# Optimization experiments

Measured on AMD Instinct MI355X. Metric: run time of the kernel, lower is better.

Reference implementation:

```python
import jax, jax.numpy as jnp
import numpy as np


def setup_inputs() -> dict:
    key = jax.random.key(0)
    ks = jax.random.split(key, 5)
    N, C, H, W = 4, 256, 64, 64
    fan_scale = 1.0 / np.sqrt(C)  # kaiming-ish scale for 1x1 conv weights
    x = jax.random.normal(ks[0], (N, C, H, W), dtype=jnp.float32)
    Wq = jax.random.normal(ks[1], (C, C), dtype=jnp.float32) * fan_scale
    Wk = jax.random.normal(ks[2], (C, C), dtype=jnp.float32) * fan_scale
    Wv = jax.random.normal(ks[3], (C, C), dtype=jnp.float32) * fan_scale
    bq = jnp.zeros((C,), dtype=jnp.float32)
    bk = jnp.zeros((C,), dtype=jnp.float32)
    bv = jnp.zeros((C,), dtype=jnp.float32)
    gamma = jax.random.uniform(ks[4], (1,), dtype=jnp.float32)
    return {"x": x, "Wq": Wq, "bq": bq, "Wk": Wk, "bk": bk, "Wv": Wv, "bv": bv, "gamma": gamma}


def reference(x, Wq, bq, Wk, bk, Wv, bv, gamma):
    # x: (N, C, H, W); 1x1 convs are channel-mixing matmuls.
    N, C, H, W = x.shape
    HW = H * W
    xf = x.reshape(N, C, HW)
    q = jnp.einsum('oc,ncl->nol', Wq, xf) + bq[None, :, None]  # (N, C, HW)
    k = jnp.einsum('oc,ncl->nol', Wk, xf) + bk[None, :, None]
    v = jnp.einsum('oc,ncl->nol', Wv, xf) + bv[None, :, None]
    # spatial mode: energy = softmax(Q^T K) over last dim (no 1/sqrt(d) scaling)
    energy = jax.nn.softmax(jnp.einsum('nci,ncj->nij', q, k), axis=-1)  # (N, HW, HW)
    # att[n,c,i] = sum_j v[n,c,j] * energy[n,i,j]  (bmm(value, energy^T))
    att = jnp.einsum('ncj,nij->nci', v, energy)  # (N, C, HW)
    # in_channels == out_channels -> residual is identity
    out = x + gamma[0] * att.reshape(N, C, H, W)
    return out
```

## Files before the change

### kernel.cpp

```cpp
#include <hip/hip_runtime.h>

typedef unsigned short ushort_t;
typedef unsigned int u32;
typedef _Float16 f16;
typedef f16 f16x8 __attribute__((ext_vector_type(8)));
typedef f16 f16x2 __attribute__((ext_vector_type(2)));
typedef ushort_t u16x8 __attribute__((ext_vector_type(8)));
typedef float f32x4 __attribute__((ext_vector_type(4)));
typedef float f32x16 __attribute__((ext_vector_type(16)));

#define C_DIM 256
#define HW 4096
#define CHW (C_DIM*HW)
#define L2E 1.4426950408889634f

__device__ __align__(16) f16 g_xbT[4 * CHW];
__device__ __align__(16) f16 g_q[4 * CHW];
__device__ __align__(16) f16 g_k[4 * CHW];
__device__ __align__(16) f16 g_v[4 * CHW];
__device__ __align__(16) f16 g_opart[16 * CHW];
__device__ __align__(16) float g_ml[16 * 2 * HW];

__device__ __forceinline__ float bf2f(ushort_t h) {
    union { u32 u; float f; } v; v.u = ((u32)h) << 16; return v.f;
}
__device__ __forceinline__ ushort_t f2bf(float f) {
    union { float f; u32 u; } v; v.f = f;
    u32 r = v.u + 0x7FFF + ((v.u >> 16) & 1);
    return (ushort_t)(r >> 16);
}
__device__ __forceinline__ float fin0(float v) {
    return (v > -1e30f && v < 1e30f) ? v : 0.f;
}
__device__ __forceinline__ f16 sf16(float v) {
    return (f16)((v > -1e4f && v < 1e4f) ? v : 0.f);
}
__device__ __forceinline__ void gl2lds16(const f16* g, f16* l) {
    __builtin_amdgcn_global_load_lds(
        (const __attribute__((address_space(1))) u32*)g,
        (__attribute__((address_space(3))) u32*)l, 16, 0, 0);
}
__device__ __forceinline__ int probe_mode(const void* p) {
    int lane = threadIdx.x & 63;
    float v = fabsf(bf2f(((const ushort_t*)p)[lane]));
    v = (v < 1e6f) ? v : 1e6f;
#pragma unroll
    for (int d = 1; d < 64; d <<= 1) v += __shfl_xor(v, d, 64);
    return (v * (1.f / 64.f) > 100.f) ? 1 : 0;
}

__global__ void k_sentinel(ushort_t* out, int n) {
    int i = blockIdx.x * 256 + threadIdx.x;
    if (i < n) out[i] = f2bf(777.f);
}

__global__ __launch_bounds__(256) void k_transpose(const void* __restrict__ xv) {
    __shared__ f16 t[64][66];
    int mode = probe_mode(xv);
    int n = blockIdx.z, c0 = blockIdx.y * 64, l0 = blockIdx.x * 64;
    int tid = threadIdx.x;
    f16* ob = g_xbT + n * CHW;
    int lq = (tid & 15) * 4;
    int cl = tid >> 4;
    if (mode == 0) {
        const ushort_t* xb = (const ushort_t*)xv + n * CHW;
#pragma unroll
        for (int p = 0; p < 4; ++p) {
            int c = cl + 16 * p;
            ushort4 v = *(const ushort4*)(xb + (c0 + c) * HW + l0 + lq);
            t[lq + 0][c] = sf16(bf2f(v.x));
            t[lq + 1][c] = sf16(bf2f(v.y));
            t[lq + 2][c] = sf16(bf2f(v.z));
            t[lq + 3][c] = sf16(bf2f(v.w));
        }
    } else {
        const float* xb = (const float*)xv + n * CHW;
#pragma unroll
        for (int p = 0; p < 4; ++p) {
            int c = cl + 16 * p;
            float4 v = *(const float4*)(xb + (c0 + c) * HW + l0 + lq);
            t[lq + 0][c] = sf16(v.x);
            t[lq + 1][c] = sf16(v.y);
            t[lq + 2][c] = sf16(v.z);
            t[lq + 3][c] = sf16(v.w);
        }
    }
    __syncthreads();
    int c2 = (tid & 31) * 2;
    int lr = tid >> 5;
#pragma unroll
    for (int p = 0; p < 8; ++p) {
        int l = lr + 8 * p;
        u32 pair = *(const u32*)&t[l][c2];
        *(u32*)(ob + (l0 + l) * C_DIM + c0 + c2) = pair;
    }
}

__global__ __launch_bounds__(256) void k_proj(
    const void* __restrict__ Wq, const void* __restrict__ bq,
    const void* __restrict__ Wk, const void* __restrict__ bk,
    const void* __restrict__ Wv, const void* __restrict__ bv)
{
    __shared__ __align__(16) f16 lds_x[128 * 64];
    __shared__ __align__(16) f16 lds_w[128 * 64];
    int l0 = blockIdx.x * 128;
    int og0 = blockIdx.y * 128;
    int n = blockIdx.z;
    int mat = og0 >> 8;
    int om0 = og0 & 255;
    const void* W = (mat == 0) ? Wq : (mat == 1) ? Wk : Wv;
    const void* bias = (mat == 0) ? bq : (mat == 1) ? bk : bv;
    int mode = probe_mode(W);
    int tid = threadIdx.x, w = tid >> 6, lane = tid & 63;
    int quad = lane >> 4, l16 = lane & 15;
    const f16* xb = g_xbT + n * CHW;

    f32x4 acc[2][8];
#pragma unroll
    for (int a = 0; a < 2; a++)
#pragma unroll
        for (int b = 0; b < 8; b++) acc[a][b] = f32x4{0.f, 0.f, 0.f, 0.f};

    for (int ch = 0; ch < 4; ++ch) {
        int cc0 = ch * 64;
        f16x8 xs[4], wsr[4];
#pragma unroll
        for (int ti = 0; ti < 4; ++ti) {
            int s = (w * 4 + ti) * 64 + lane;
            int row = s >> 3, gp = s & 7;
            xs[ti] = *(const f16x8*)(xb + (l0 + row) * C_DIM + cc0 + gp * 8);
            f16x8 h;
            if (mode == 0) {
                u16x8 wv = *(const u16x8*)((const ushort_t*)W + (om0 + row) * C_DIM + cc0 + gp * 8);
#pragma unroll
                for (int e = 0; e < 8; e++) h[e] = sf16(bf2f(wv[e]));
            } else {
                const float* wf = (const float*)W + (om0 + row) * C_DIM + cc0 + gp * 8;
#pragma unroll
                for (int e = 0; e < 8; e++) h[e] = sf16(wf[e]);
            }
            wsr[ti] = h;
        }
        __syncthreads();
#pragma unroll
        for (int ti = 0; ti < 4; ++ti) {
            int s = (w * 4 + ti) * 64 + lane;
            int row = s >> 3, gp = s & 7;
            int pos = gp ^ (row & 7);
            *(f16x8*)(lds_x + (row * 8 + pos) * 8) = xs[ti];
            *(f16x8*)(lds_w + (row * 8 + pos) * 8) = wsr[ti];
        }
        __syncthreads();
#pragma unroll
        for (int ks = 0; ks < 2; ++ks) {
            f16x8 af[2];
#pragma unroll
            for (int mt = 0; mt < 2; ++mt) {
                int row = w * 32 + mt * 16 + l16;
                int g = ks * 4 + quad;
                int pos = g ^ (row & 7);
                af[mt] = *(const f16x8*)(lds_x + (row * 8 + pos) * 8);
            }
#pragma unroll
            for (int nt = 0; nt < 8; ++nt) {
                int rowo = nt * 16 + l16;
                int g = ks * 4 + quad;
                int pos = g ^ (rowo & 7);
                f16x8 bfv = *(const f16x8*)(lds_w + (rowo * 8 + pos) * 8);
                if (mat < 2) {
                    acc[0][nt] = __builtin_amdgcn_mfma_f32_16x16x32_f16(af[0], bfv, acc[0][nt], 0, 0, 0);
                    acc[1][nt] = __builtin_amdgcn_mfma_f32_16x16x32_f16(af[1], bfv, acc[1][nt], 0, 0, 0);
                } else {
                    acc[0][nt] = __builtin_amdgcn_mfma_f32_16x16x32_f16(bfv, af[0], acc[0][nt], 0, 0, 0);
                    acc[1][nt] = __builtin_amdgcn_mfma_f32_16x16x32_f16(bfv, af[1], acc[1][nt], 0, 0, 0);
                }
            }
        }
        __syncthreads();
    }

    auto loadb = [&](int i) -> float {
        return mode ? ((const float*)bias)[i] : bf2f(((const ushort_t*)bias)[i]);
    };
    if (mat < 2) {
        f16* T = ((mat == 0) ? g_q : g_k) + n * CHW;
        float bvv[8];
#pragma unroll
        for (int nt = 0; nt < 8; nt++) bvv[nt] = loadb(om0 + nt * 16 + l16);
#pragma unroll
        for (int mt = 0; mt < 2; mt++)
#pragma unroll
            for (int nt = 0; nt < 8; nt++)
#pragma unroll
                for (int r = 0; r < 4; r++) {
                    int l = l0 + w * 32 + mt * 16 + quad * 4 + r;
                    int o = om0 + nt * 16 + l16;
                    T[l * C_DIM + o] = sf16(acc[mt][nt][r] + bvv[nt]);
                }
    } else {
        f16* T = g_v + n * CHW;
#pragma unroll
        for (int mt = 0; mt < 2; mt++)
#pragma unroll
            for (int nt = 0; nt < 8; nt++)
#pragma unroll
                for (int r = 0; r < 4; r++) {
                    int o = om0 + nt * 16 + quad * 4 + r;
                    int l = l0 + w * 32 + mt * 16 + l16;
                    T[o * HW + l] = sf16(acc[mt][nt][r] + loadb(o));
                }
    }
}

__device__ __forceinline__ f16x8 pack_pfrag(const float* p, int h) {
    union PK { u32 u; f16x2 h2; } t0, t1, t2, t3;
    t0.h2 = f16x2{(f16)p[0], (f16)p[1]};
    t1.h2 = f16x2{(f16)p[2], (f16)p[3]};
    t2.h2 = f16x2{(f16)p[4], (f16)p[5]};
    t3.h2 = f16x2{(f16)p[6], (f16)p[7]};
    u32 sa = __shfl_xor(t0.u, 32, 64);
    u32 sb = __shfl_xor(t1.u, 32, 64);
    u32 sc = __shfl_xor(t2.u, 32, 64);
    u32 sd = __shfl_xor(t3.u, 32, 64);
    union RW { u32 w[4]; f16x8 v; } r;
    r.w[0] = h ? sc : t0.u;
    r.w[1] = h ? sd : t1.u;
    r.w[2] = h ? t2.u : sa;
    r.w[3] = h ? t3.u : sb;
    return r.v;
}

__global__ __launch_bounds__(256, 2) void k_attn() {
    __shared__ __align__(16) f16 smem[40960];
    f16* kbuf = smem;
    f16* vbuf = smem + 16384;

    int bid = blockIdx.x;
    int x8 = bid & 7;
    int n = x8 >> 1, jhi = x8 & 1;
    int rest = bid >> 3;
    int jlo = rest & 1;
    int i0 = (rest >> 1) * 128;
    int jq = jhi * 2 + jlo;
    int tid = threadIdx.x, w = tid >> 6, lane = tid & 63;
    int j5 = lane & 31, h = lane >> 5;

    const f16* Qb = g_q + n * CHW;
    const f16* Kb = g_k + n * CHW;
    const f16* Vb = g_v + n * CHW;

    f16x8 qf[16];
    {
        const f16* qrow = Qb + (i0 + w * 32 + j5) * C_DIM + h * 8;
#pragma unroll
        for (int ck = 0; ck < 16; ++ck)
            qf[ck] = *(const f16x8*)(qrow + ck * 16);
    }

    int k_lane = h * 256 + j5 * 8;
    int v_lane = h * 2048 + j5 * 8;

    const f16* ksrc = Kb + (jq * 1024 + j5) * C_DIM + (w * 2 + h) * 8;
    const f16* vsrc = Vb + tid * HW + jq * 1024;
    int dst_w = w * 512;

    f32x16 o_acc[8];
#pragma unroll
    for (int ct = 0; ct < 8; ++ct)
#pragma unroll
        for (int r = 0; r < 16; ++r) o_acc[ct][r] = 0.f;

    float m_ = -1e30f, l_ = 0.f, al_prev = 1.f;
    f16x8 pf0 = {}, pf1 = {};

#pragma unroll
    for (int s = 0; s < 4; ++s) gl2lds16(ksrc + s * 64, kbuf + s * 2048 + dst_w);
    ksrc += 32 * C_DIM;
#pragma unroll
    for (int s = 0; s < 4; ++s) gl2lds16(vsrc + s * 8, vbuf + s * 2048 + dst_w);
    vsrc += 32;
    __syncthreads();

    int vs_stage = 1, vs_pv = 2;
    for (int it = 0; it < 32; ++it) {
        int kb_cur = it & 1;
        if (it < 31) {
#pragma unroll
            for (int s = 0; s < 4; ++s)
                gl2lds16(ksrc + s * 64, kbuf + (kb_cur ^ 1) * 8192 + s * 2048 + dst_w);
            ksrc += 32 * C_DIM;
#pragma unroll
            for (int s = 0; s < 4; ++s)
                gl2lds16(vsrc + s * 8, vbuf + vs_stage * 8192 + s * 2048 + dst_w);
            vsrc += 32;
        }

        const f16* kb = kbuf + kb_cur * 8192 + k_lane;
        f32x16 st;
#pragma unroll
        for (int r = 0; r < 16; ++r) st[r] = 0.f;
        __builtin_amdgcn_s_setprio(1);
#pragma unroll
        for (int ck = 0; ck < 16; ++ck) {
            f16x8 kf = *(const f16x8*)(kb + ck * 512);
            st = __builtin_amdgcn_mfma_f32_32x32x16_f16(kf, qf[ck], st, 0, 0, 0);
        }

        if (it > 0) {
            if (__any(al_prev < 1.f)) {
#pragma unroll
                for (int ct = 0; ct < 8; ++ct)
#pragma unroll
                    for (int r = 0; r < 16; ++r) o_acc[ct][r] *= al_prev;
            }
            const f16* vb = vbuf + vs_pv * 8192 + v_lane;
#pragma unroll
            for (int ct = 0; ct < 8; ++ct) {
                f16x8 v0 = *(const f16x8*)(vb + ct * 256);
                f16x8 v1 = *(const f16x8*)(vb + 4096 + ct * 256);
                o_acc[ct] = __builtin_amdgcn_mfma_f32_32x32x16_f16(v0, pf0, o_acc[ct], 0, 0, 0);
                o_acc[ct] = __builtin_amdgcn_mfma_f32_32x32x16_f16(v1, pf1, o_acc[ct], 0, 0, 0);
            }
        }
        __builtin_amdgcn_s_setprio(0);

        float mx0 = fmaxf(fmaxf(st[0], st[1]), fmaxf(st[2], st[3]));
        float mx1 = fmaxf(fmaxf(st[4], st[5]), fmaxf(st[6], st[7]));
        float mx2 = fmaxf(fmaxf(st[8], st[9]), fmaxf(st[10], st[11]));
        float mx3 = fmaxf(fmaxf(st[12], st[13]), fmaxf(st[14], st[15]));
        float smax = fmaxf(fmaxf(mx0, mx1), fmaxf(mx2, mx3));
        smax = fmaxf(smax, __shfl_xor(smax, 32, 64));
        float mq = __builtin_ceilf(smax * 0.125f) * 8.f;
        float mn = fmaxf(m_, mq);
        float al = __builtin_amdgcn_exp2f((m_ - mn) * L2E);
        float nl = -mn * L2E;
        float p[16];
#pragma unroll
        for (int r = 0; r < 16; ++r)
            p[r] = __builtin_amdgcn_exp2f(st[r] * L2E + nl);
        float a0 = (p[0] + p[1]) + (p[2] + p[3]);
        float a1 = (p[4] + p[5]) + (p[6] + p[7]);
        float a2 = (p[8] + p[9]) + (p[10] + p[11]);
        float a3 = (p[12] + p[13]) + (p[14] + p[15]);
        float rs = (a0 + a1) + (a2 + a3);
        rs += __shfl_xor(rs, 32, 64);
        m_ = mn;
        l_ = l_ * al + rs;
        al_prev = al;
        pf0 = pack_pfrag(p, h);
        pf1 = pack_pfrag(p + 8, h);

        __syncthreads();
        vs_pv = (vs_pv == 2) ? 0 : vs_pv + 1;
        vs_stage = (vs_stage == 2) ? 0 : vs_stage + 1;
    }

    {
        if (__any(al_prev < 1.f)) {
#pragma unroll
            for (int ct = 0; ct < 8; ++ct)
#pragma unroll
                for (int r = 0; r < 16; ++r) o_acc[ct][r] *= al_prev;
        }
        const f16* vb = vbuf + vs_pv * 8192 + v_lane;
#pragma unroll
        for (int ct = 0; ct < 8; ++ct) {
            f16x8 v0 = *(const f16x8*)(vb + ct * 256);
            f16x8 v1 = *(const f16x8*)(vb + 4096 + ct * 256);
            o_acc[ct] = __builtin_amdgcn_mfma_f32_32x32x16_f16(v0, pf0, o_acc[ct], 0, 0, 0);
            o_acc[ct] = __builtin_amdgcn_mfma_f32_32x32x16_f16(v1, pf1, o_acc[ct], 0, 0, 0);
        }
    }

    int slot = jq * 4 + n;
    int i_out = i0 + w * 32 + j5;
    if (h == 0) {
        g_ml[(slot * 2 + 0) * HW + i_out] = m_;
        g_ml[(slot * 2 + 1) * HW + i_out] = l_;
    }
    float inv = (l_ > 1e-30f) ? 1.f / l_ : 0.f;
    f16* ob = g_opart + slot * CHW + i_out;
#pragma unroll
    for (int ct = 0; ct < 8; ++ct) {
        int cbase = ct * 32 + 4 * h;
#pragma unroll
        for (int r = 0; r < 16; ++r) {
            int c = cbase + (r & 3) + 8 * (r >> 2);
            ob[c * HW] = (f16)(o_acc[ct][r] * inv);
        }
    }
}

__global__ __launch_bounds__(256) void k_combine(
    const void* __restrict__ xv, const void* __restrict__ gv, void* __restrict__ outv)
{
    int mode = probe_mode(xv);
    float gam = fin0(mode ? ((const float*)gv)[0] : bf2f(((const ushort_t*)gv)[0]));
    int n = blockIdx.y;
    int off = blockIdx.x * 2048 + threadIdx.x * 8;
    int i = off & (HW - 1);

    u16x8 op[4];
    float ms[4][8], ls[4][8];
#pragma unroll
    for (int s = 0; s < 4; ++s) {
        int slot = s * 4 + n;
        op[s] = *(const u16x8*)((const ushort_t*)g_opart + slot * CHW + off);
        float4 mA = *(const float4*)&g_ml[(slot * 2 + 0) * HW + i];
        float4 mB = *(const float4*)&g_ml[(slot * 2 + 0) * HW + i + 4];
        float4 lA = *(const float4*)&g_ml[(slot * 2 + 1) * HW + i];
        float4 lB = *(const float4*)&g_ml[(slot * 2 + 1) * HW + i + 4];
        ms[s][0]=mA.x; ms[s][1]=mA.y; ms[s][2]=mA.z; ms[s][3]=mA.w;
        ms[s][4]=mB.x; ms[s][5]=mB.y; ms[s][6]=mB.z; ms[s][7]=mB.w;
        ls[s][0]=lA.x; ls[s][1]=lA.y; ls[s][2]=lA.z; ls[s][3]=lA.w;
        ls[s][4]=lB.x; ls[s][5]=lB.y; ls[s][6]=lB.z; ls[s][7]=lB.w;
    }

    float o[8];
#pragma unroll
    for (int e = 0; e < 8; ++e) {
        float m = fmaxf(fmaxf(ms[0][e], ms[1][e]), fmaxf(ms[2][e], ms[3][e]));
        float num = 0.f, den = 0.f;
#pragma unroll
        for (int s = 0; s < 4; ++s) {
            float wgt = __builtin_amdgcn_exp2f((ms[s][e] - m) * L2E) * ls[s][e];
            union { ushort_t u; f16 h; } cv; cv.u = (ushort_t)op[s][e];
            num += wgt * (float)cv.h;
            den += wgt;
        }
        o[e] = (den > 1e-30f) ? num / den : 0.f;
    }

    if (mode == 0) {
        u16x8 xp = *(const u16x8*)((const ushort_t*)xv + n * CHW + off);
        u16x8 res;
#pragma unroll
        for (int e = 0; e < 8; ++e)
            res[e] = f2bf(fin0(bf2f((ushort_t)xp[e]) + gam * o[e]));
        *(u16x8*)((ushort_t*)outv + n * CHW + off) = res;
    } else {
        const float* xb = (const float*)xv + n * CHW + off;
        float* outb = (float*)outv + n * CHW + off;
        float4 xA = *(const float4*)xb;
        float4 xB = *(const float4*)(xb + 4);
        float4 rA, rB;
        rA.x = fin0(xA.x + gam * o[0]); rA.y = fin0(xA.y + gam * o[1]);
        rA.z = fin0(xA.z + gam * o[2]); rA.w = fin0(xA.w + gam * o[3]);
        rB.x = fin0(xB.x + gam * o[4]); rB.y = fin0(xB.y + gam * o[5]);
        rB.z = fin0(xB.z + gam * o[6]); rB.w = fin0(xB.w + gam * o[7]);
        *(float4*)outb = rA;
        *(float4*)(outb + 4) = rB;
    }
}

extern "C" void kernel_launch(void* const* d_in, const int* in_sizes, int n_in,
                              void* d_out, int out_size, void* d_ws, size_t ws_size,
                              hipStream_t stream) {
    (void)d_ws; (void)ws_size;
    bool ok = (n_in == 8) &&
              in_sizes[0] == 4 * CHW &&
              in_sizes[1] == C_DIM * C_DIM && in_sizes[2] == C_DIM &&
              in_sizes[3] == C_DIM * C_DIM && in_sizes[4] == C_DIM &&
              in_sizes[5] == C_DIM * C_DIM && in_sizes[6] == C_DIM &&
              in_sizes[7] == 1 && out_size == 4 * CHW;
    if (!ok) {
        hipLaunchKernelGGL(k_sentinel, dim3((out_size + 255) / 256), dim3(256), 0, stream,
                           (ushort_t*)d_out, out_size);
        return;
    }
    hipLaunchKernelGGL(k_transpose, dim3(64, 4, 4), dim3(256), 0, stream, d_in[0]);
    hipLaunchKernelGGL(k_proj, dim3(32, 6, 4), dim3(256), 0, stream,
                       d_in[1], d_in[2], d_in[3], d_in[4], d_in[5], d_in[6]);
    hipLaunchKernelGGL(k_attn, dim3(512), dim3(256), 0, stream);
    hipLaunchKernelGGL(k_combine, dim3(CHW / 2048, 4), dim3(256), 0, stream,
                       d_in[0], d_in[7], d_out);
}
```

Baseline: 239.9 us.

## Interleave QK and PV MFMAs per step with double-buffered V tiles

The attention loop now issues the QK^T MFMAs and the previous step's PV MFMAs interleaved in a single loop. The score accumulator is split into two independent chains that are summed afterwards. The V staging buffer drops from three stages to two, shrinking LDS, and the V load now happens in the same iteration as its tile is consumed one step later. The cross-half row-sum shuffle moves out of the loop and runs once at the end. The aim is to hide MFMA dependency latency and cut per-iteration shuffle work, at the cost of higher register pressure and less slack between V loads and their use.

New measurement: 239.3 us. Within noise of the previous version (-0.2%).

```diff
diff --git a/kernel.cpp b/kernel.cpp
--- a/kernel.cpp
+++ b/kernel.cpp
@@ -231,7 +231,7 @@
 }
 
 __global__ __launch_bounds__(256, 2) void k_attn() {
-    __shared__ __align__(16) f16 smem[40960];
+    __shared__ __align__(16) f16 smem[32768];
     f16* kbuf = smem;
     f16* vbuf = smem + 16384;
 
@@ -276,53 +276,56 @@
 #pragma unroll
     for (int s = 0; s < 4; ++s) gl2lds16(ksrc + s * 64, kbuf + s * 2048 + dst_w);
     ksrc += 32 * C_DIM;
-#pragma unroll
-    for (int s = 0; s < 4; ++s) gl2lds16(vsrc + s * 8, vbuf + s * 2048 + dst_w);
-    vsrc += 32;
     __syncthreads();
 
-    int vs_stage = 1, vs_pv = 2;
     for (int it = 0; it < 32; ++it) {
-        int kb_cur = it & 1;
+        int kcur = it & 1;
         if (it < 31) {
 #pragma unroll
             for (int s = 0; s < 4; ++s)
-                gl2lds16(ksrc + s * 64, kbuf + (kb_cur ^ 1) * 8192 + s * 2048 + dst_w);
+                gl2lds16(ksrc + s * 64, kbuf + (kcur ^ 1) * 8192 + s * 2048 + dst_w);
             ksrc += 32 * C_DIM;
-#pragma unroll
-            for (int s = 0; s < 4; ++s)
-                gl2lds16(vsrc + s * 8, vbuf + vs_stage * 8192 + s * 2048 + dst_w);
-            vsrc += 32;
-        }
-
-        const f16* kb = kbuf + kb_cur * 8192 + k_lane;
+        }
+#pragma unroll
+        for (int s = 0; s < 4; ++s)
+            gl2lds16(vsrc + s * 8, vbuf + (it & 1) * 8192 + s * 2048 + dst_w);
+        vsrc += 32;
+
+        if (it > 0 && __any(al_prev < 1.f)) {
+#pragma unroll
+            for (int ct = 0; ct < 8; ++ct)
+#pragma unroll
+                for (int r = 0; r < 16; ++r) o_acc[ct][r] *= al_prev;
+        }
+
+        const f16* kb = kbuf + kcur * 8192 + k_lane;
+        f32x16 sa, sb;
+#pragma unroll
+        for (int r = 0; r < 16; ++r) { sa[r] = 0.f; sb[r] = 0.f; }
+        __builtin_amdgcn_s_setprio(1);
+        if (it > 0) {
+            const f16* vb = vbuf + ((it - 1) & 1) * 8192 + v_lane;
+#pragma unroll
+            for (int ck = 0; ck < 16; ++ck) {
+                f16x8 kf = *(const f16x8*)(kb + ck * 512);
+                if (ck & 1) sb = __builtin_amdgcn_mfma_f32_32x32x16_f16(kf, qf[ck], sb, 0, 0, 0);
+                else        sa = __builtin_amdgcn_mfma_f32_32x32x16_f16(kf, qf[ck], sa, 0, 0, 0);
+                f16x8 vf = *(const f16x8*)(vb + (ck & 1) * 4096 + (ck >> 1) * 256);
+                o_acc[ck >> 1] = __builtin_amdgcn_mfma_f32_32x32x16_f16(
+                    vf, (ck & 1) ? pf1 : pf0, o_acc[ck >> 1], 0, 0, 0);
+            }
+        } else {
+#pragma unroll
+            for (int ck = 0; ck < 16; ++ck) {
+                f16x8 kf = *(const f16x8*)(kb + ck * 512);
+                if (ck & 1) sb = __builtin_amdgcn_mfma_f32_32x32x16_f16(kf, qf[ck], sb, 0, 0, 0);
+                else        sa = __builtin_amdgcn_mfma_f32_32x32x16_f16(kf, qf[ck], sa, 0, 0, 0);
+            }
+        }
+        __builtin_amdgcn_s_setprio(0);
         f32x16 st;
 #pragma unroll
-        for (int r = 0; r < 16; ++r) st[r] = 0.f;
-        __builtin_amdgcn_s_setprio(1);
-#pragma unroll
-        for (int ck = 0; ck < 16; ++ck) {
-            f16x8 kf = *(const f16x8*)(kb + ck * 512);
-            st = __builtin_amdgcn_mfma_f32_32x32x16_f16(kf, qf[ck], st, 0, 0, 0);
-        }
-
-        if (it > 0) {
-            if (__any(al_prev < 1.f)) {
-#pragma unroll
-                for (int ct = 0; ct < 8; ++ct)
-#pragma unroll
-                    for (int r = 0; r < 16; ++r) o_acc[ct][r] *= al_prev;
-            }
-            const f16* vb = vbuf + vs_pv * 8192 + v_lane;
-#pragma unroll
-            for (int ct = 0; ct < 8; ++ct) {
-                f16x8 v0 = *(const f16x8*)(vb + ct * 256);
-                f16x8 v1 = *(const f16x8*)(vb + 4096 + ct * 256);
-                o_acc[ct] = __builtin_amdgcn_mfma_f32_32x32x16_f16(v0, pf0, o_acc[ct], 0, 0, 0);
-                o_acc[ct] = __builtin_amdgcn_mfma_f32_32x32x16_f16(v1, pf1, o_acc[ct], 0, 0, 0);
-            }
-        }
-        __builtin_amdgcn_s_setprio(0);
+        for (int r = 0; r < 16; ++r) st[r] = sa[r] + sb[r];
 
         float mx0 = fmaxf(fmaxf(st[0], st[1]), fmaxf(st[2], st[3]));
         float mx1 = fmaxf(fmaxf(st[4], st[5]), fmaxf(st[6], st[7]));
@@ -343,7 +346,6 @@
         float a2 = (p[8] + p[9]) + (p[10] + p[11]);
         float a3 = (p[12] + p[13]) + (p[14] + p[15]);
         float rs = (a0 + a1) + (a2 + a3);
-        rs += __shfl_xor(rs, 32, 64);
         m_ = mn;
         l_ = l_ * al + rs;
         al_prev = al;
@@ -351,8 +353,6 @@
         pf1 = pack_pfrag(p + 8, h);
 
         __syncthreads();
-        vs_pv = (vs_pv == 2) ? 0 : vs_pv + 1;
-        vs_stage = (vs_stage == 2) ? 0 : vs_stage + 1;
     }
 
     {
@@ -362,7 +362,7 @@
 #pragma unroll
                 for (int r = 0; r < 16; ++r) o_acc[ct][r] *= al_prev;
         }
-        const f16* vb = vbuf + vs_pv * 8192 + v_lane;
+        const f16* vb = vbuf + 8192 + v_lane;
 #pragma unroll
         for (int ct = 0; ct < 8; ++ct) {
             f16x8 v0 = *(const f16x8*)(vb + ct * 256);
@@ -371,6 +371,8 @@
             o_acc[ct] = __builtin_amdgcn_mfma_f32_32x32x16_f16(v1, pf1, o_acc[ct], 0, 0, 0);
         }
     }
+
+    l_ += __shfl_xor(l_, 32, 64);
 
     int slot = jq * 4 + n;
     int i_out = i0 + w * 32 + j5;
```

## Split attention channel dimension across wave pairs with LDS score exchange

Applied to the files above, without the earlier changes.

Each block now covers 64 query rows instead of 128, with pairs of waves splitting the 256 channels: each wave computes a partial QK^T over 128 channels, swaps partial scores with its peer through LDS, and accumulates PV for only half of the output channels. This halves the per-wave register footprint (qf and o_acc), which allows three blocks per CU, and doubles the grid size to improve occupancy and latency hiding. K and V staging drops from double/triple buffering to single buffers with explicit waitcnt and barriers, trading pipelining depth and extra synchronisation for lower LDS use. K/V are fetched once per 64 query rows instead of 128, so global and L2 traffic rises.

Measured after the change: 288.6 us. 20.3% more time.

```diff
diff --git a/kernel.cpp b/kernel.cpp
--- a/kernel.cpp
+++ b/kernel.cpp
@@ -230,43 +230,44 @@
     return r.v;
 }
 
-__global__ __launch_bounds__(256, 2) void k_attn() {
-    __shared__ __align__(16) f16 smem[40960];
+__global__ __launch_bounds__(256, 3) void k_attn() {
+    __shared__ __align__(16) f16 smem[24576];
     f16* kbuf = smem;
-    f16* vbuf = smem + 16384;
+    f16* vbuf = smem + 8192;
+    float* xbuf = (float*)(smem + 16384);
 
     int bid = blockIdx.x;
-    int x8 = bid & 7;
-    int n = x8 >> 1, jhi = x8 & 1;
-    int rest = bid >> 3;
-    int jlo = rest & 1;
-    int i0 = (rest >> 1) * 128;
-    int jq = jhi * 2 + jlo;
+    int n = bid & 3;
+    int jq = (bid >> 2) & 3;
+    int i0 = (bid >> 4) * 64;
     int tid = threadIdx.x, w = tid >> 6, lane = tid & 63;
     int j5 = lane & 31, h = lane >> 5;
+    int ic = w >> 1, ch = w & 1;
 
     const f16* Qb = g_q + n * CHW;
     const f16* Kb = g_k + n * CHW;
     const f16* Vb = g_v + n * CHW;
 
-    f16x8 qf[16];
+    f16x8 qf[8];
     {
-        const f16* qrow = Qb + (i0 + w * 32 + j5) * C_DIM + h * 8;
-#pragma unroll
-        for (int ck = 0; ck < 16; ++ck)
+        const f16* qrow = Qb + (i0 + ic * 32 + j5) * C_DIM + ch * 128 + h * 8;
+#pragma unroll
+        for (int ck = 0; ck < 8; ++ck)
             qf[ck] = *(const f16x8*)(qrow + ck * 16);
     }
 
-    int k_lane = h * 256 + j5 * 8;
-    int v_lane = h * 2048 + j5 * 8;
+    int k_lane = ch * 4096 + h * 256 + j5 * 8;
+    int v_lane = h * 2048 + ch * 1024 + j5 * 8;
+    float* x_my = xbuf + (ic * 2 + ch) * 1024 + lane * 16;
+    const float* x_peer = xbuf + (ic * 2 + (ch ^ 1)) * 1024 + lane * 16;
 
     const f16* ksrc = Kb + (jq * 1024 + j5) * C_DIM + (w * 2 + h) * 8;
     const f16* vsrc = Vb + tid * HW + jq * 1024;
     int dst_w = w * 512;
 
-    f32x16 o_acc[8];
-#pragma unroll
-    for (int ct = 0; ct < 8; ++ct)
+    f32x16 o_acc[4];
+#pragma unroll
+    for (int ct = 0; ct < 4; ++ct)
 #pragma unroll
         for (int r = 0; r < 16; ++r) o_acc[ct][r] = 0.f;
 
@@ -276,54 +277,71 @@
 #pragma unroll
     for (int s = 0; s < 4; ++s) gl2lds16(ksrc + s * 64, kbuf + s * 2048 + dst_w);
     ksrc += 32 * C_DIM;
-#pragma unroll
-    for (int s = 0; s < 4; ++s) gl2lds16(vsrc + s * 8, vbuf + s * 2048 + dst_w);
-    vsrc += 32;
-    __syncthreads();
-
-    int vs_stage = 1, vs_pv = 2;
+    asm volatile("s_waitcnt vmcnt(0)" ::: "memory");
+    __builtin_amdgcn_s_barrier();
+    __builtin_amdgcn_sched_barrier(0);
+
     for (int it = 0; it < 32; ++it) {
-        int kb_cur = it & 1;
+        if (it > 0) {
+            asm volatile("s_waitcnt vmcnt(4)" ::: "memory");
+            __builtin_amdgcn_s_barrier();
+            __builtin_amdgcn_sched_barrier(0);
+        }
+
+        const f16* kb = kbuf + k_lane;
+        f32x16 sp;
+#pragma unroll
+        for (int r = 0; r < 16; ++r) sp[r] = 0.f;
+        __builtin_amdgcn_s_setprio(1);
+#pragma unroll
+        for (int ck = 0; ck < 8; ++ck) {
+            f16x8 kf = *(const f16x8*)(kb + ck * 512);
+            sp = __builtin_amdgcn_mfma_f32_32x32x16_f16(kf, qf[ck], sp, 0, 0, 0);
+        }
+        __builtin_amdgcn_s_setprio(0);
+#pragma unroll
+        for (int q = 0; q < 4; ++q)
+            *(f32x4*)(x_my + q * 4) = f32x4{sp[q*4+0], sp[q*4+1], sp[q*4+2], sp[q*4+3]};
+        asm volatile("s_waitcnt lgkmcnt(0)" ::: "memory");
+
+        asm volatile("s_waitcnt vmcnt(0)" ::: "memory");
+        __builtin_amdgcn_s_barrier();
+        __builtin_amdgcn_sched_barrier(0);
+
         if (it < 31) {
 #pragma unroll
             for (int s = 0; s < 4; ++s)
-                gl2lds16(ksrc + s * 64, kbuf + (kb_cur ^ 1) * 8192 + s * 2048 + dst_w);
+                gl2lds16(ksrc + s * 64, kbuf + s * 2048 + dst_w);
             ksrc += 32 * C_DIM;
-#pragma unroll
-            for (int s = 0; s < 4; ++s)
-                gl2lds16(vsrc + s * 8, vbuf + vs_stage * 8192 + s * 2048 + dst_w);
-            vsrc += 32;
-        }
-
-        const f16* kb = kbuf + kb_cur * 8192 + k_lane;
-        f32x16 st;
-#pragma unroll
-        for (int r = 0; r < 16; ++r) st[r] = 0.f;
-        __builtin_amdgcn_s_setprio(1);
-#pragma unroll
-        for (int ck = 0; ck < 16; ++ck) {
-            f16x8 kf = *(const f16x8*)(kb + ck * 512);
-            st = __builtin_amdgcn_mfma_f32_32x32x16_f16(kf, qf[ck], st, 0, 0, 0);
-        }
+        }
+        __builtin_amdgcn_sched_barrier(0);
 
         if (it > 0) {
             if (__any(al_prev < 1.f)) {
 #pragma unroll
-                for (int ct = 0; ct < 8; ++ct)
+                for (int ct = 0; ct < 4; ++ct)
 #pragma unroll
                     for (int r = 0; r < 16; ++r) o_acc[ct][r] *= al_prev;
             }
-            const f16* vb = vbuf + vs_pv * 8192 + v_lane;
-#pragma unroll
-            for (int ct = 0; ct < 8; ++ct) {
+            const f16* vb = vbuf + v_lane;
+            __builtin_amdgcn_s_setprio(1);
+#pragma unroll
+            for (int ct = 0; ct < 4; ++ct) {
                 f16x8 v0 = *(const f16x8*)(vb + ct * 256);
                 f16x8 v1 = *(const f16x8*)(vb + 4096 + ct * 256);
                 o_acc[ct] = __builtin_amdgcn_mfma_f32_32x32x16_f16(v0, pf0, o_acc[ct], 0, 0, 0);
                 o_acc[ct] = __builtin_amdgcn_mfma_f32_32x32x16_f16(v1, pf1, o_acc[ct], 0, 0, 0);
             }
-        }
-        __builtin_amdgcn_s_setprio(0);
-
+            __builtin_amdgcn_s_setprio(0);
+        }
+
+        f32x16 st;
+#pragma unroll
+        for (int q = 0; q < 4; ++q) {
+            f32x4 pp = *(const f32x4*)(x_peer + q * 4);
+#pragma unroll
+            for (int e = 0; e < 4; ++e) st[q*4+e] = sp[q*4+e] + pp[e];
+        }
         float mx0 = fmaxf(fmaxf(st[0], st[1]), fmaxf(st[2], st[3]));
         float mx1 = fmaxf(fmaxf(st[4], st[5]), fmaxf(st[6], st[7]));
         float mx2 = fmaxf(fmaxf(st[8], st[9]), fmaxf(st[10], st[11]));
@@ -343,28 +361,34 @@
         float a2 = (p[8] + p[9]) + (p[10] + p[11]);
         float a3 = (p[12] + p[13]) + (p[14] + p[15]);
         float rs = (a0 + a1) + (a2 + a3);
-        rs += __shfl_xor(rs, 32, 64);
         m_ = mn;
         l_ = l_ * al + rs;
         al_prev = al;
         pf0 = pack_pfrag(p, h);
         pf1 = pack_pfrag(p + 8, h);
 
-        __syncthreads();
-        vs_pv = (vs_pv == 2) ? 0 : vs_pv + 1;
-        vs_stage = (vs_stage == 2) ? 0 : vs_stage + 1;
-    }
-
+        __builtin_amdgcn_s_barrier();
+        __builtin_amdgcn_sched_barrier(0);
+#pragma unroll
+        for (int s = 0; s < 4; ++s)
+            gl2lds16(vsrc + s * 8, vbuf + s * 2048 + dst_w);
+        vsrc += 32;
+        __builtin_amdgcn_sched_barrier(0);
+    }
+
+    asm volatile("s_waitcnt vmcnt(0)" ::: "memory");
+    __builtin_amdgcn_s_barrier();
+    __builtin_amdgcn_sched_barrier(0);
     {
         if (__any(al_prev < 1.f)) {
 #pragma unroll
-            for (int ct = 0; ct < 8; ++ct)
+            for (int ct = 0; ct < 4; ++ct)
 #pragma unroll
                 for (int r = 0; r < 16; ++r) o_acc[ct][r] *= al_prev;
         }
-        const f16* vb = vbuf + vs_pv * 8192 + v_lane;
-#pragma unroll
-        for (int ct = 0; ct < 8; ++ct) {
+        const f16* vb = vbuf + v_lane;
+#pragma unroll
+        for (int ct = 0; ct < 4; ++ct) {
             f16x8 v0 = *(const f16x8*)(vb + ct * 256);
             f16x8 v1 = *(const f16x8*)(vb + 4096 + ct * 256);
             o_acc[ct] = __builtin_amdgcn_mfma_f32_32x32x16_f16(v0, pf0, o_acc[ct], 0, 0, 0);
@@ -372,17 +396,19 @@
         }
     }
 
+    l_ += __shfl_xor(l_, 32, 64);
+
     int slot = jq * 4 + n;
-    int i_out = i0 + w * 32 + j5;
-    if (h == 0) {
+    int i_out = i0 + ic * 32 + j5;
+    if (h == 0 && ch == 0) {
         g_ml[(slot * 2 + 0) * HW + i_out] = m_;
         g_ml[(slot * 2 + 1) * HW + i_out] = l_;
     }
     float inv = (l_ > 1e-30f) ? 1.f / l_ : 0.f;
     f16* ob = g_opart + slot * CHW + i_out;
 #pragma unroll
-    for (int ct = 0; ct < 8; ++ct) {
-        int cbase = ct * 32 + 4 * h;
+    for (int ct = 0; ct < 4; ++ct) {
+        int cbase = ch * 128 + ct * 32 + 4 * h;
 #pragma unroll
         for (int r = 0; r < 16; ++r) {
             int c = cbase + (r & 3) + 8 * (r >> 2);
@@ -471,7 +497,7 @@
     hipLaunchKernelGGL(k_transpose, dim3(64, 4, 4), dim3(256), 0, stream, d_in[0]);
     hipLaunchKernelGGL(k_proj, dim3(32, 6, 4), dim3(256), 0, stream,
                        d_in[1], d_in[2], d_in[3], d_in[4], d_in[5], d_in[6]);
-    hipLaunchKernelGGL(k_attn, dim3(512), dim3(256), 0, stream);
+    hipLaunchKernelGGL(k_attn, dim3(1024), dim3(256), 0, stream);
     hipLaunchKernelGGL(k_combine, dim3(CHW / 2048, 4), dim3(256), 0, stream,
                        d_in[0], d_in[7], d_out);
 }
```
